# Performance work log

Hardware: AMD Instinct MI355X
Metric: run time of the kernel (lower is better)

The kernel has to match this reference:

```python
import jax, jax.numpy as jnp
import numpy as np

HEADS = 12
D_MODEL = 768
D_K = D_MODEL // HEADS


def setup_inputs() -> dict:
    key = jax.random.key(0)
    ks = jax.random.split(key, 5)
    B, S = 2, 2048
    scale = 1.0 / np.sqrt(D_MODEL)
    return {
        "q": jax.random.normal(ks[0], (B, S, D_MODEL), dtype=jnp.float32),
        "k": jax.random.normal(ks[1], (B, S, D_MODEL), dtype=jnp.float32),
        "v": jax.random.normal(ks[2], (B, S, D_MODEL), dtype=jnp.float32),
        "Wk": jax.random.normal(ks[3], (D_MODEL, D_MODEL), dtype=jnp.float32) * scale,
        "bk": jnp.zeros((D_MODEL,), dtype=jnp.float32),
        "Wo": jax.random.normal(ks[4], (D_MODEL, D_MODEL), dtype=jnp.float32) * scale,
        "bo": jnp.zeros((D_MODEL,), dtype=jnp.float32),
    }


def reference(q, k, v, Wk, bk, Wo, bo):
    B, S, _ = q.shape
    # NOTE: faithful to source bug: q, k, v ALL projected with k_linear.
    def proj(x):
        y = x @ Wk.T + bk                    # [B,S,D]
        return y.reshape(B, -1, HEADS, D_K).transpose(0, 2, 1, 3)  # [B,H,S,Dk]

    qh, kh, vh = proj(q), proj(k), proj(v)
    scores = jnp.einsum('bhsd,bhtd->bhst', qh, kh) / jnp.sqrt(jnp.float32(D_K))
    attn = jax.nn.softmax(scores, axis=-1)   # dropout is identity in eval
    out = jnp.einsum('bhst,bhtd->bhsd', attn, vh)
    concat = out.transpose(0, 2, 1, 3).reshape(B, -1, D_MODEL)
    return concat @ Wo.T + bo
```

## Files before the change

### kernel.cpp

```cpp
#include <hip/hip_runtime.h>
#include <hip/hip_bf16.h>
#include <stddef.h>

#define HEADS 12
#define DM 768
#define DK 64
#define SEQ 2048
#define NB 2
#define WSZ (DM * DM)
#define QSCALE 0.18033688011112043f

typedef __attribute__((ext_vector_type(8))) short short8;
typedef __attribute__((ext_vector_type(4))) float f32x4;
typedef __attribute__((ext_vector_type(16))) float f32x16;

#define MFMA16(A, B, C) __builtin_amdgcn_mfma_f32_16x16x32_bf16((A), (B), (C), 0, 0, 0)
#define MFMA32(A, B, C) __builtin_amdgcn_mfma_f32_32x32x16_bf16((A), (B), (C), 0, 0, 0)

__device__ __forceinline__ unsigned short f2bf(float x) {
  union { float f; unsigned u; } c;
  c.f = x;
  unsigned r = (c.u + 0x7FFFu + ((c.u >> 16) & 1u)) >> 16;
  return (unsigned short)r;
}
__device__ __forceinline__ float bf2f(unsigned short h) {
  union { float f; unsigned u; } c;
  c.u = ((unsigned)h) << 16;
  return c.f;
}

__device__ __forceinline__ void async16(const void* g, void* l) {
  __builtin_amdgcn_global_load_lds(
      (const __attribute__((address_space(1))) void*)g,
      (__attribute__((address_space(3))) void*)l, 16, 0, 0);
}

__device__ __forceinline__ void splitpk(float a, float b, unsigned& hu, unsigned& lu) {
  union { __hip_bfloat162 v; unsigned u; } c;
  c.v = __float22bfloat162_rn(make_float2(a, b));
  hu = c.u;
  const float ra = a - bf2f((unsigned short)(hu & 0xFFFFu));
  const float rb = b - bf2f((unsigned short)(hu >> 16));
  c.v = __float22bfloat162_rn(make_float2(ra, rb));
  lu = c.u;
}
__device__ __forceinline__ unsigned pk2bf(float a, float b) {
  union { __hip_bfloat162 v; unsigned u; } c;
  c.v = __float22bfloat162_rn(make_float2(a, b));
  return c.u;
}

__device__ __forceinline__ void pl32swap(unsigned& a, unsigned& b) {
  auto r = __builtin_amdgcn_permlane32_swap(a, b, false, false);
  a = r[0];
  b = r[1];
}


__global__ __launch_bounds__(256) void prep_split(
    const float* __restrict__ q, const float* __restrict__ k,
    const float* __restrict__ v, const float* __restrict__ Wk,
    const float* __restrict__ Wo, unsigned short* __restrict__ xq,
    unsigned short* __restrict__ xk, unsigned short* __restrict__ xv,
    unsigned short* __restrict__ wkh, unsigned short* __restrict__ wkl,
    unsigned short* __restrict__ woh, unsigned short* __restrict__ wol) {
  __shared__ __align__(16) unsigned short Lh[64 * 136];
  __shared__ __align__(16) unsigned short Ll[64 * 136];
  const int tid = threadIdx.x;
  int id = blockIdx.x;
  const float* S;
  unsigned short *H, *L = nullptr;
  int RT, RT16;
  if (id < 1152) {
    S = (id < 384) ? q : (id < 768) ? k : v;
    H = (id < 384) ? xq : (id < 768) ? xk : xv;
    id = id % 384; RT = 64; RT16 = 256;
  } else if (id < 1224) {
    S = Wk; H = wkh; L = wkl; id -= 1152; RT = 12; RT16 = 48;
  } else {
    S = Wo; H = woh; L = wol; id -= 1224; RT = 12; RT16 = 48;
  }
  const int rb = id % RT, kb = id / RT;
  const int mlane = tid >> 4;
  const int klane = (tid & 15) * 8;

#pragma unroll
  for (int rr = 0; rr < 4; ++rr) {
    const int m = rr * 16 + mlane;
    const float* src = &S[(size_t)(rb * 64 + m) * DM + kb * 128 + klane];
    float a[8];
    *(float4*)&a[0] = *(const float4*)&src[0];
    *(float4*)&a[4] = *(const float4*)&src[4];
    if (L) {
      unsigned hu[4], lu[4];
#pragma unroll
      for (int u = 0; u < 4; ++u) splitpk(a[2 * u], a[2 * u + 1], hu[u], lu[u]);
      *(uint4*)&Lh[m * 136 + klane] = *(uint4*)&hu[0];
      *(uint4*)&Ll[m * 136 + klane] = *(uint4*)&lu[0];
    } else {
      unsigned hu[4];
#pragma unroll
      for (int u = 0; u < 4; ++u) hu[u] = pk2bf(a[2 * u], a[2 * u + 1]);
      *(uint4*)&Lh[m * 136 + klane] = *(uint4*)&hu[0];
    }
  }
  __syncthreads();

  const int t = tid >> 4;
  const int ktp = t >> 2, mtp = t & 3;
  const size_t gt = ((size_t)(kb * 4 + ktp) * RT16 + (rb * 4 + mtp)) * 512;
#pragma unroll
  for (int i = 0; i < 4; ++i) {
    const int c = i * 16 + (tid & 15);
    const int lsrc = (mtp * 16 + (tid & 15)) * 136 + ktp * 32 + i * 8;
    *(uint4*)&H[gt + c * 8] = *(uint4*)&Lh[lsrc];
    if (L) *(uint4*)&L[gt + c * 8] = *(uint4*)&Ll[lsrc];
  }
}

__global__ __launch_bounds__(256, 3) void gemm_proj(
    const unsigned short* __restrict__ Xq, const unsigned short* __restrict__ Xk,
    const unsigned short* __restrict__ Xv, const unsigned short* __restrict__ Bh_,
    const unsigned short* __restrict__ Bl_, const float* __restrict__ bias,
    unsigned short* __restrict__ q_h, unsigned short* __restrict__ q_l,
    unsigned short* __restrict__ k_h, unsigned short* __restrict__ vt_h) {
  __shared__ __align__(16) unsigned short Ash[16 * 512];
  __shared__ __align__(16) unsigned short Bsh[12 * 512];
  __shared__ __align__(16) unsigned short Bsl[12 * 512];

  const int tid = threadIdx.x, z = blockIdx.z;
  const unsigned short* __restrict__ A = (z == 0) ? Xq : (z == 1) ? Xk : Xv;
  const int id = blockIdx.x;
  const int mt0 = (id & 31) * 8, nt0 = (id >> 5) * 6;
  const int lane = tid & 63, wv = tid >> 6;
  const int l15 = lane & 15, quad = lane >> 4;
  const int wm = (wv >> 1) * 4, wn = (wv & 1) * 3;
  const int lx = lane * 8;

  f32x4 acc[4][3];
#pragma unroll
  for (int i = 0; i < 4; ++i)
#pragma unroll
    for (int j = 0; j < 3; ++j) acc[i][j] = (f32x4){0.f, 0.f, 0.f, 0.f};

  for (int kk = 0; kk < 12; ++kk) {
    const int k2 = kk * 2;
    __syncthreads();
    async16(&A[((size_t)k2 * 256 + mt0 + wv) * 512 + lx], &Ash[wv * 512]);
    async16(&A[((size_t)k2 * 256 + mt0 + wv + 4) * 512 + lx],
            &Ash[(wv + 4) * 512]);
    async16(&A[((size_t)(k2 + 1) * 256 + mt0 + wv) * 512 + lx],
            &Ash[(8 + wv) * 512]);
    async16(&A[((size_t)(k2 + 1) * 256 + mt0 + wv + 4) * 512 + lx],
            &Ash[(12 + wv) * 512]);
#pragma unroll
    for (int i = 0; i < 3; ++i) {
      const int t = wv + 4 * i;
      const int ks = t / 6, nt = t % 6;
      async16(&Bh_[((size_t)(k2 + ks) * 48 + nt0 + nt) * 512 + lx],
              &Bsh[t * 512]);
      async16(&Bl_[((size_t)(k2 + ks) * 48 + nt0 + nt) * 512 + lx],
              &Bsl[t * 512]);
    }
    __syncthreads();

#pragma unroll
    for (int ks = 0; ks < 2; ++ks) {
      short8 bh8[3], bl8[3];
#pragma unroll
      for (int nt = 0; nt < 3; ++nt) {
        bh8[nt] = *(const short8*)&Bsh[(ks * 6 + wn + nt) * 512 + lx];
        bl8[nt] = *(const short8*)&Bsl[(ks * 6 + wn + nt) * 512 + lx];
      }
#pragma unroll
      for (int mt = 0; mt < 4; ++mt) {
        const short8 ah8 = *(const short8*)&Ash[(ks * 8 + wm + mt) * 512 + lx];
#pragma unroll
        for (int nt = 0; nt < 3; ++nt) {
          acc[mt][nt] = MFMA16(ah8, bh8[nt], acc[mt][nt]);
          acc[mt][nt] = MFMA16(ah8, bl8[nt], acc[mt][nt]);
        }
      }
    }
  }

#pragma unroll
  for (int mt = 0; mt < 4; ++mt)
#pragma unroll
    for (int nt = 0; nt < 3; ++nt) {
      const int n = (nt0 + wn + nt) * 16 + l15;
      const float bv = bias[n];
      const int hh = n >> 6, dk = n & 63;
#pragma unroll
      for (int j = 0; j < 4; ++j) {
        const int m = (mt0 + wm + mt) * 16 + quad * 4 + j;
        const int b = m >> 11, t = m & 2047;
        const int bh = b * HEADS + hh;
        if (z == 0) {
          const float y = (acc[mt][nt][j] + bv) * QSCALE;
          const unsigned short yh = f2bf(y);
          const int a = (bh * SEQ + t) * DK + dk;
          q_h[a] = yh;
          q_l[a] = f2bf(y - bf2f(yh));
        } else if (z == 1) {
          const int a = bh * 131072 + (t >> 5) * 2048 + (dk >> 4) * 512 +
                        ((t & 31) + ((dk & 15) >> 3) * 32) * 8 + (dk & 7);
          k_h[a] = f2bf(acc[mt][nt][j] + bv);
        } else {
          const int a = bh * 131072 + (t >> 4) * 1024 + (dk >> 5) * 512 +
                        ((dk & 31) + ((t & 15) >> 3) * 32) * 8 + (t & 7);
          vt_h[a] = f2bf(acc[mt][nt][j] + bv);
        }
      }
    }
}

__global__ __launch_bounds__(256, 2) void gemm_out(
    const unsigned short* __restrict__ Ah_, const unsigned short* __restrict__ Al_,
    const unsigned short* __restrict__ Bh_, const unsigned short* __restrict__ Bl_,
    const float* __restrict__ bias, float* __restrict__ outF) {
  __shared__ __align__(16) unsigned short Ash[8 * 512];
  __shared__ __align__(16) unsigned short Asl[8 * 512];
  __shared__ __align__(16) unsigned short Bsh[12 * 512];
  __shared__ __align__(16) unsigned short Bsl[12 * 512];

  const int tid = threadIdx.x, id = blockIdx.x;
  const int mt0 = (id & 63) * 4, nt0 = (id >> 6) * 6;
  const int lane = tid & 63, wv = tid >> 6;
  const int l15 = lane & 15, quad = lane >> 4;
  const int wm = (wv >> 1) * 2, wn = (wv & 1) * 3;
  const int lx = lane * 8;

  f32x4 acc[2][3];
#pragma unroll
  for (int i = 0; i < 2; ++i)
#pragma unroll
    for (int j = 0; j < 3; ++j) acc[i][j] = (f32x4){0.f, 0.f, 0.f, 0.f};

  for (int kk = 0; kk < 12; ++kk) {
    const int k2 = kk * 2;
    __syncthreads();
#pragma unroll
    for (int ks = 0; ks < 2; ++ks) {
      async16(&Ah_[((size_t)(k2 + ks) * 256 + mt0 + wv) * 512 + lx],
              &Ash[(ks * 4 + wv) * 512]);
      async16(&Al_[((size_t)(k2 + ks) * 256 + mt0 + wv) * 512 + lx],
              &Asl[(ks * 4 + wv) * 512]);
    }
#pragma unroll
    for (int i = 0; i < 3; ++i) {
      const int t = wv + 4 * i;
      const int ks = t / 6, nt = t % 6;
      async16(&Bh_[((size_t)(k2 + ks) * 48 + nt0 + nt) * 512 + lx],
              &Bsh[t * 512]);
      async16(&Bl_[((size_t)(k2 + ks) * 48 + nt0 + nt) * 512 + lx],
              &Bsl[t * 512]);
    }
    __syncthreads();

#pragma unroll
    for (int ks = 0; ks < 2; ++ks) {
      short8 bh8[3], bl8[3];
#pragma unroll
      for (int nt = 0; nt < 3; ++nt) {
        bh8[nt] = *(const short8*)&Bsh[(ks * 6 + wn + nt) * 512 + lx];
        bl8[nt] = *(const short8*)&Bsl[(ks * 6 + wn + nt) * 512 + lx];
      }
#pragma unroll
      for (int mt = 0; mt < 2; ++mt) {
        const short8 ah8 = *(const short8*)&Ash[(ks * 4 + wm + mt) * 512 + lx];
        const short8 al8 = *(const short8*)&Asl[(ks * 4 + wm + mt) * 512 + lx];
#pragma unroll
        for (int nt = 0; nt < 3; ++nt) {
          acc[mt][nt] = MFMA16(ah8, bh8[nt], acc[mt][nt]);
          acc[mt][nt] = MFMA16(al8, bh8[nt], acc[mt][nt]);
          acc[mt][nt] = MFMA16(ah8, bl8[nt], acc[mt][nt]);
        }
      }
    }
  }

#pragma unroll
  for (int mt = 0; mt < 2; ++mt)
#pragma unroll
    for (int nt = 0; nt < 3; ++nt) {
      const int n = (nt0 + wn + nt) * 16 + l15;
      const float bv = bias[n];
#pragma unroll
      for (int j = 0; j < 4; ++j) {
        const int m = (mt0 + wm + mt) * 16 + quad * 4 + j;
        outF[(size_t)m * DM + n] = acc[mt][nt][j] + bv;
      }
    }
}

__global__ __launch_bounds__(256, 3) void attn_mfma(
    const unsigned short* __restrict__ q_h, const unsigned short* __restrict__ q_l,
    const unsigned short* __restrict__ k_h, const unsigned short* __restrict__ vt_h,
    unsigned short* __restrict__ cch, unsigned short* __restrict__ ccl) {
  __shared__ __align__(16) union {
    unsigned short stage[32 * 512];
    float osh[64 * 64];
  } sm;
  __shared__ float Lred[4][32];

  const int tid = threadIdx.x, lane = tid & 63, wv = tid >> 6;
  const int l31 = lane & 31, hi = lane >> 5;
  const int qh = wv & 1, th = wv >> 1;
  const int id = blockIdx.x;
  const int bh = id % 24, q0 = (id / 24) << 6;
  const int lx = lane * 8;

  short8 Qf[4][2];
#pragma unroll
  for (int ks = 0; ks < 4; ++ks) {
    const int off = (bh * SEQ + q0 + qh * 32 + l31) * DK + ks * 16 + hi * 8;
    Qf[ks][0] = *(const short8*)&q_h[off];
    Qf[ks][1] = *(const short8*)&q_l[off];
  }

  f32x16 O[2];
#pragma unroll
  for (int i = 0; i < 2; ++i)
#pragma unroll
    for (int r = 0; r < 16; ++r) O[i][r] = 0.f;
  float lsum = 0.f;

  const unsigned short* __restrict__ kbh = k_h + (size_t)bh * 131072;
  const unsigned short* __restrict__ vbh = vt_h + (size_t)bh * 131072;
  unsigned short* const Ks = &sm.stage[0];
  unsigned short* const Vs = &sm.stage[16 * 512];

  for (int t0 = 0; t0 < SEQ; t0 += 128) {
    __syncthreads();
#pragma unroll
    for (int dt = 0; dt < 4; ++dt)
      async16(&kbh[((size_t)(t0 >> 5) + wv) * 2048 + dt * 512 + lx],
              &Ks[(wv * 4 + dt) * 512]);
#pragma unroll
    for (int i = 0; i < 2; ++i)
#pragma unroll
      for (int dt = 0; dt < 2; ++dt)
        async16(&vbh[((size_t)(t0 >> 4) + wv * 2 + i) * 1024 + dt * 512 + lx],
                &Vs[((wv * 2 + i) * 2 + dt) * 512]);
    __syncthreads();

    f32x16 St[2];
#pragma unroll
    for (int i = 0; i < 2; ++i)
#pragma unroll
      for (int r = 0; r < 16; ++r) St[i][r] = 0.f;
    __builtin_amdgcn_s_setprio(1);
#pragma unroll
    for (int tt = 0; tt < 2; ++tt)
#pragma unroll
      for (int ks = 0; ks < 4; ++ks) {
        const short8 kh8 =
            *(const short8*)&Ks[((th * 2 + tt) * 4 + ks) * 512 + lx];
        St[tt] = MFMA32(kh8, Qf[ks][0], St[tt]);
        St[tt] = MFMA32(kh8, Qf[ks][1], St[tt]);
      }
    __builtin_amdgcn_s_setprio(0);

#pragma unroll
    for (int tt = 0; tt < 2; ++tt) {
      float s = 0.f;
#pragma unroll
      for (int r = 0; r < 16; ++r) {
        St[tt][r] = __builtin_amdgcn_exp2f(St[tt][r]);
        s += St[tt][r];
      }
      lsum += s;
    }

    short8 pa[4];
#pragma unroll
    for (int tt = 0; tt < 2; ++tt)
#pragma unroll
      for (int c = 0; c < 2; ++c) {
        unsigned a0 = pk2bf(St[tt][c * 8 + 0], St[tt][c * 8 + 1]);
        unsigned a1 = pk2bf(St[tt][c * 8 + 2], St[tt][c * 8 + 3]);
        unsigned b0 = pk2bf(St[tt][c * 8 + 4], St[tt][c * 8 + 5]);
        unsigned b1 = pk2bf(St[tt][c * 8 + 6], St[tt][c * 8 + 7]);
        pl32swap(a0, b0);
        pl32swap(a1, b1);
        unsigned w[4] = {a0, a1, b0, b1};
        pa[tt * 2 + c] = *(short8*)&w[0];
      }

    __builtin_amdgcn_s_setprio(1);
#pragma unroll
    for (int tc = 0; tc < 4; ++tc) {
#pragma unroll
      for (int dt = 0; dt < 2; ++dt) {
        const short8 vb8 =
            *(const short8*)&Vs[((th * 4 + tc) * 2 + dt) * 512 + lx];
        O[dt] = MFMA32(pa[tc], vb8, O[dt]);
      }
    }
    __builtin_amdgcn_s_setprio(0);
  }

  {
    float l = lsum + __shfl_xor(lsum, 32);
    if (lane < 32) Lred[wv][lane] = l;
  }
  asm volatile("s_waitcnt vmcnt(0)" ::: "memory");
  __syncthreads();
  if (th == 1) {
#pragma unroll
    for (int dt = 0; dt < 2; ++dt)
#pragma unroll
      for (int r = 0; r < 16; ++r) {
        const int qloc = (r & 3) + 8 * (r >> 2) + 4 * hi;
        sm.osh[(qh * 32 + qloc) * 64 + dt * 32 + l31] = O[dt][r];
      }
  }
  __syncthreads();
  if (th == 0) {
    const int b = bh / HEADS, hh = bh % HEADS;
#pragma unroll
    for (int dt = 0; dt < 2; ++dt)
#pragma unroll
      for (int r = 0; r < 16; ++r) {
        const int qloc = (r & 3) + 8 * (r >> 2) + 4 * hi;
        const float inv = 1.0f / (Lred[qh][qloc] + Lred[qh + 2][qloc]);
        const float y =
            (O[dt][r] + sm.osh[(qh * 32 + qloc) * 64 + dt * 32 + l31]) * inv;
        const int m = b * SEQ + q0 + qh * 32 + qloc;
        const int kk = hh * 64 + dt * 32 + l31;
        const int a = ((kk >> 5) * 256 + (m >> 4)) * 512 +
                      (((kk & 31) >> 3) * 16 + (m & 15)) * 8 + (kk & 7);
        const unsigned short yh = f2bf(y);
        cch[a] = yh;
        ccl[a] = f2bf(y - bf2f(yh));
      }
  }
}

extern "C" void kernel_launch(void* const* d_in, const int* in_sizes, int n_in,
                              void* d_out, int out_size, void* d_ws,
                              size_t ws_size, hipStream_t stream) {
  const float* q = (const float*)d_in[0];
  const float* k = (const float*)d_in[1];
  const float* v = (const float*)d_in[2];
  const float* Wk = (const float*)d_in[3];
  const float* bk = (const float*)d_in[4];
  const float* Wo = (const float*)d_in[5];
  const float* bo = (const float*)d_in[6];
  float* out = (float*)d_out;

  const size_t SZ = (size_t)NB * SEQ * DM;
  unsigned short* ws16 = (unsigned short*)d_ws;
  unsigned short* xq = ws16;
  unsigned short* xk = ws16 + SZ;
  unsigned short* xv = ws16 + 2 * SZ;
  unsigned short* cch = xq;
  unsigned short* ccl = xk;
  unsigned short* qp_h = ws16 + 3 * SZ;
  unsigned short* qp_l = ws16 + 4 * SZ;
  unsigned short* kp = ws16 + 5 * SZ;
  unsigned short* vtp = ws16 + 6 * SZ;
  unsigned short* wkh = ws16 + 7 * SZ;
  unsigned short* wkl = wkh + WSZ;
  unsigned short* woh = wkl + WSZ;
  unsigned short* wol = woh + WSZ;

  prep_split<<<dim3(1296), 256, 0, stream>>>(q, k, v, Wk, Wo, xq, xk, xv, wkh,
                                             wkl, woh, wol);
  gemm_proj<<<dim3(256, 1, 3), 256, 0, stream>>>(xq, xk, xv, wkh, wkl, bk,
                                                 qp_h, qp_l, kp, vtp);
  attn_mfma<<<dim3(768), 256, 0, stream>>>(qp_h, qp_l, kp, vtp, cch, ccl);
  gemm_out<<<dim3(512), 256, 0, stream>>>(cch, ccl, woh, wol, bo, out);
}
```

Measured before the change: 191.9 us.

## Split attention key range across eight waves per block instead of four

Doubles the attention block to 512 threads so each wave handles 32 keys of every 128-key tile instead of 64. K loads now go to the first four waves and V loads to the other four. Partial outputs from three key-slices are reduced through a larger shared-memory buffer. The aim is more waves in flight to hide MFMA and exp latency. The cost is a bigger LDS footprint (48KB for osh), a heavier final reduction, and fewer MFMAs per wave between barriers.

```diff
diff --git a/kernel.cpp b/kernel.cpp
--- a/kernel.cpp
+++ b/kernel.cpp
@@ -294,15 +294,15 @@
     }
 }
 
-__global__ __launch_bounds__(256, 3) void attn_mfma(
+__global__ __launch_bounds__(512, 4) void attn_mfma(
     const unsigned short* __restrict__ q_h, const unsigned short* __restrict__ q_l,
     const unsigned short* __restrict__ k_h, const unsigned short* __restrict__ vt_h,
     unsigned short* __restrict__ cch, unsigned short* __restrict__ ccl) {
   __shared__ __align__(16) union {
     unsigned short stage[32 * 512];
-    float osh[64 * 64];
+    float osh[3 * 64 * 64];
   } sm;
-  __shared__ float Lred[4][32];
+  __shared__ float Lred[8][32];
 
   const int tid = threadIdx.x, lane = tid & 63, wv = tid >> 6;
   const int l31 = lane & 31, hi = lane >> 5;
@@ -333,68 +333,65 @@
 
   for (int t0 = 0; t0 < SEQ; t0 += 128) {
     __syncthreads();
-#pragma unroll
-    for (int dt = 0; dt < 4; ++dt)
-      async16(&kbh[((size_t)(t0 >> 5) + wv) * 2048 + dt * 512 + lx],
-              &Ks[(wv * 4 + dt) * 512]);
-#pragma unroll
-    for (int i = 0; i < 2; ++i)
-#pragma unroll
-      for (int dt = 0; dt < 2; ++dt)
-        async16(&vbh[((size_t)(t0 >> 4) + wv * 2 + i) * 1024 + dt * 512 + lx],
-                &Vs[((wv * 2 + i) * 2 + dt) * 512]);
-    __syncthreads();
-
-    f32x16 St[2];
-#pragma unroll
-    for (int i = 0; i < 2; ++i)
-#pragma unroll
-      for (int r = 0; r < 16; ++r) St[i][r] = 0.f;
+    if (wv < 4) {
+#pragma unroll
+      for (int dt = 0; dt < 4; ++dt)
+        async16(&kbh[((size_t)(t0 >> 5) + wv) * 2048 + dt * 512 + lx],
+                &Ks[(wv * 4 + dt) * 512]);
+    } else {
+      const int w2 = wv - 4;
+#pragma unroll
+      for (int i = 0; i < 2; ++i)
+#pragma unroll
+        for (int dt = 0; dt < 2; ++dt)
+          async16(
+              &vbh[((size_t)(t0 >> 4) + w2 * 2 + i) * 1024 + dt * 512 + lx],
+              &Vs[((w2 * 2 + i) * 2 + dt) * 512]);
+    }
+    __syncthreads();
+
+    f32x16 St;
+#pragma unroll
+    for (int r = 0; r < 16; ++r) St[r] = 0.f;
     __builtin_amdgcn_s_setprio(1);
 #pragma unroll
-    for (int tt = 0; tt < 2; ++tt)
-#pragma unroll
-      for (int ks = 0; ks < 4; ++ks) {
-        const short8 kh8 =
-            *(const short8*)&Ks[((th * 2 + tt) * 4 + ks) * 512 + lx];
-        St[tt] = MFMA32(kh8, Qf[ks][0], St[tt]);
-        St[tt] = MFMA32(kh8, Qf[ks][1], St[tt]);
-      }
+    for (int ks = 0; ks < 4; ++ks) {
+      const short8 kh8 = *(const short8*)&Ks[(th * 4 + ks) * 512 + lx];
+      St = MFMA32(kh8, Qf[ks][0], St);
+      St = MFMA32(kh8, Qf[ks][1], St);
+    }
     __builtin_amdgcn_s_setprio(0);
 
-#pragma unroll
-    for (int tt = 0; tt < 2; ++tt) {
+    {
       float s = 0.f;
 #pragma unroll
       for (int r = 0; r < 16; ++r) {
-        St[tt][r] = __builtin_amdgcn_exp2f(St[tt][r]);
-        s += St[tt][r];
+        St[r] = __builtin_amdgcn_exp2f(St[r]);
+        s += St[r];
       }
       lsum += s;
     }
 
-    short8 pa[4];
-#pragma unroll
-    for (int tt = 0; tt < 2; ++tt)
-#pragma unroll
-      for (int c = 0; c < 2; ++c) {
-        unsigned a0 = pk2bf(St[tt][c * 8 + 0], St[tt][c * 8 + 1]);
-        unsigned a1 = pk2bf(St[tt][c * 8 + 2], St[tt][c * 8 + 3]);
-        unsigned b0 = pk2bf(St[tt][c * 8 + 4], St[tt][c * 8 + 5]);
-        unsigned b1 = pk2bf(St[tt][c * 8 + 6], St[tt][c * 8 + 7]);
-        pl32swap(a0, b0);
-        pl32swap(a1, b1);
-        unsigned w[4] = {a0, a1, b0, b1};
-        pa[tt * 2 + c] = *(short8*)&w[0];
-      }
+    short8 pa[2];
+#pragma unroll
+    for (int c = 0; c < 2; ++c) {
+      unsigned a0 = pk2bf(St[c * 8 + 0], St[c * 8 + 1]);
+      unsigned a1 = pk2bf(St[c * 8 + 2], St[c * 8 + 3]);
+      unsigned b0 = pk2bf(St[c * 8 + 4], St[c * 8 + 5]);
+      unsigned b1 = pk2bf(St[c * 8 + 6], St[c * 8 + 7]);
+      pl32swap(a0, b0);
+      pl32swap(a1, b1);
+      unsigned w[4] = {a0, a1, b0, b1};
+      pa[c] = *(short8*)&w[0];
+    }
 
     __builtin_amdgcn_s_setprio(1);
 #pragma unroll
-    for (int tc = 0; tc < 4; ++tc) {
+    for (int tc = 0; tc < 2; ++tc) {
 #pragma unroll
       for (int dt = 0; dt < 2; ++dt) {
         const short8 vb8 =
-            *(const short8*)&Vs[((th * 4 + tc) * 2 + dt) * 512 + lx];
+            *(const short8*)&Vs[((th * 2 + tc) * 2 + dt) * 512 + lx];
         O[dt] = MFMA32(pa[tc], vb8, O[dt]);
       }
     }
@@ -407,13 +404,14 @@
   }
   asm volatile("s_waitcnt vmcnt(0)" ::: "memory");
   __syncthreads();
-  if (th == 1) {
+  if (th > 0) {
+    float* slab = &sm.osh[(th - 1) * 4096];
 #pragma unroll
     for (int dt = 0; dt < 2; ++dt)
 #pragma unroll
       for (int r = 0; r < 16; ++r) {
         const int qloc = (r & 3) + 8 * (r >> 2) + 4 * hi;
-        sm.osh[(qh * 32 + qloc) * 64 + dt * 32 + l31] = O[dt][r];
+        slab[(qh * 32 + qloc) * 64 + dt * 32 + l31] = O[dt][r];
       }
   }
   __syncthreads();
@@ -424,9 +422,12 @@
 #pragma unroll
       for (int r = 0; r < 16; ++r) {
         const int qloc = (r & 3) + 8 * (r >> 2) + 4 * hi;
-        const float inv = 1.0f / (Lred[qh][qloc] + Lred[qh + 2][qloc]);
-        const float y =
-            (O[dt][r] + sm.osh[(qh * 32 + qloc) * 64 + dt * 32 + l31]) * inv;
+        const float inv = 1.0f / (Lred[qh][qloc] + Lred[qh + 2][qloc] +
+                                  Lred[qh + 4][qloc] + Lred[qh + 6][qloc]);
+        const int oidx = (qh * 32 + qloc) * 64 + dt * 32 + l31;
+        const float y = (O[dt][r] + sm.osh[oidx] + sm.osh[4096 + oidx] +
+                         sm.osh[8192 + oidx]) *
+                        inv;
         const int m = b * SEQ + q0 + qh * 32 + qloc;
         const int kk = hh * 64 + dt * 32 + l31;
         const int a = ((kk >> 5) * 256 + (m >> 4)) * 512 +
@@ -470,6 +471,6 @@
                                              wkl, woh, wol);
   gemm_proj<<<dim3(256, 1, 3), 256, 0, stream>>>(xq, xk, xv, wkh, wkl, bk,
                                                  qp_h, qp_l, kp, vtp);
-  attn_mfma<<<dim3(768), 256, 0, stream>>>(qp_h, qp_l, kp, vtp, cch, ccl);
+  attn_mfma<<<dim3(768), 512, 0, stream>>>(qp_h, qp_l, kp, vtp, cch, ccl);
   gemm_out<<<dim3(512), 256, 0, stream>>>(cch, ccl, woh, wol, bo, out);
 }
```

Result: slower. 243.0 us (+26.6%).
